# Kernel tuning notes

Measured on AMD Instinct MI355X. Metric: run time of the kernel, lower is better.

The kernel has to match this reference:

```python
import jax, jax.numpy as jnp
import numpy as np

B, L, D = 2, 2048, 512
DI, N, K, R = 1024, 16, 4, 32  # d_inner=2*d_model, d_state, d_conv, dt_rank=ceil(512/16)
CK = 31   # conformer depthwise kernel
DFF = 2048  # feedforward_factor * d_hidden

def _ln(h, g, b):
    m = h.mean(-1, keepdims=True)
    v = ((h - m) ** 2).mean(-1, keepdims=True)
    return (h - m) * jax.lax.rsqrt(v + 1e-5) * g + b

def _dwconv(h, w, b, pad):
    # h: [B,L,C], w: [C,1,K] depthwise kernel
    y = jax.lax.conv_general_dilated(h.transpose(0, 2, 1), w, (1,), [pad],
                                     feature_group_count=h.shape[-1],
                                     dimension_numbers=('NCH', 'OIH', 'NCH'))
    return y.transpose(0, 2, 1) + b

def setup_inputs():
    key = jax.random.key(0)
    ks = jax.random.split(key, 16)
    nrm = lambda k, s, sc=0.02: jax.random.normal(k, s, jnp.float32) * sc
    return {
        'x': jax.random.normal(ks[0], (B, L, D), jnp.float32),
        'ln_g': jnp.ones(D), 'ln_b': jnp.zeros(D),
        'W_in': nrm(ks[1], (D, 2 * DI)),
        'conv_w': nrm(ks[2], (DI, 1, K), 0.1), 'conv_b': jnp.zeros(DI),
        'W_x': nrm(ks[3], (DI, R + 2 * N)),
        'W_dt': nrm(ks[4], (R, DI), 0.1), 'b_dt': nrm(ks[5], (DI,), 0.1),
        'A_log': jnp.log(jnp.broadcast_to(jnp.arange(1, N + 1, dtype=jnp.float32), (DI, N))),
        'Dp': jnp.ones(DI),
        'W_out': nrm(ks[6], (DI, D)),
        'cm_ln_g': jnp.ones(D), 'cm_ln_b': jnp.zeros(D),
        'cm_pw1_w': nrm(ks[7], (D, 2 * D)), 'cm_pw1_b': jnp.zeros(2 * D),
        'cm_dw_w': nrm(ks[8], (D, 1, CK), 0.1), 'cm_dw_b': jnp.zeros(D),
        'cm_pw2_w': nrm(ks[9], (D, D)), 'cm_pw2_b': jnp.zeros(D),
        'ff_W1': nrm(ks[10], (D, DFF)), 'ff_b1': jnp.zeros(DFF),
        'ff_W2': nrm(ks[11], (DFF, D)), 'ff_b2': jnp.zeros(D),
    }

def _forward(x, ln_g, ln_b, W_in, conv_w, conv_b, W_x, W_dt, b_dt, A_log, Dp, W_out,
             cm_ln_g, cm_ln_b, cm_pw1_w, cm_pw1_b, cm_dw_w, cm_dw_b, cm_pw2_w, cm_pw2_b,
             ff_W1, ff_b1, ff_W2, ff_b2):
    # --- pre LayerNorm ---
    h = _ln(x, ln_g, ln_b)
    # --- Mamba block ---
    xz = h @ W_in                       # [B,L,2*DI]
    xi, z = xz[..., :DI], xz[..., DI:]
    xc = jax.nn.silu(_dwconv(xi, conv_w, conv_b, (K - 1, 0)))  # causal depthwise conv
    dbl = xc @ W_x                      # [B,L,R+2N]
    dt, Bm, Cm = dbl[..., :R], dbl[..., R:R + N], dbl[..., R + N:]
    delta = jax.nn.softplus(dt @ W_dt + b_dt)           # [B,L,DI]
    A = -jnp.exp(A_log)                                  # [DI,N]
    dA = jnp.exp(delta[..., None] * A)                   # [B,L,DI,N]
    dBu = (delta * xc)[..., None] * Bm[:, :, None, :]    # [B,L,DI,N]
    def step(hs, inp):
        a, bu, c = inp
        hs = a * hs + bu                                 # [B,DI,N]
        return hs, jnp.einsum('bdn,bn->bd', hs, c)
    h0 = jnp.zeros((x.shape[0], DI, N), x.dtype)
    _, ys = jax.lax.scan(step, h0, (dA.transpose(1, 0, 2, 3), dBu.transpose(1, 0, 2, 3), Cm.transpose(1, 0, 2)))
    y = ys.transpose(1, 0, 2) + Dp * xc
    y = y * jax.nn.silu(z)
    m = y @ W_out                                        # [B,L,D]
    # --- Conformer-style conv module (residual) ---
    c = _ln(m, cm_ln_g, cm_ln_b)
    c = c @ cm_pw1_w + cm_pw1_b
    a_, g_ = jnp.split(c, 2, axis=-1)
    c = a_ * jax.nn.sigmoid(g_)  # GLU
    c = jax.nn.silu(_dwconv(c, cm_dw_w, cm_dw_b, ((CK - 1) // 2, (CK - 1) // 2)))
    c = c @ cm_pw2_w + cm_pw2_b
    m = m + c
    # --- post LayerNorm (shared params) + FFN (residual) ---
    f = _ln(m, ln_g, ln_b)
    out = f + (jax.nn.gelu(f @ ff_W1 + ff_b1) @ ff_W2 + ff_b2)
    return out

def reference(x, ln_g, ln_b, W_in, conv_w, conv_b, W_x, W_dt, b_dt, A_log, Dp, W_out,
              cm_ln_g, cm_ln_b, cm_pw1_w, cm_pw1_b, cm_dw_w, cm_dw_b, cm_pw2_w, cm_pw2_b,
              ff_W1, ff_b1, ff_W2, ff_b2):
    return _forward(x, ln_g, ln_b, W_in, conv_w, conv_b, W_x, W_dt, b_dt, A_log, Dp, W_out,
                    cm_ln_g, cm_ln_b, cm_pw1_w, cm_pw1_b, cm_dw_w, cm_dw_b, cm_pw2_w, cm_pw2_b,
                    ff_W1, ff_b1, ff_W2, ff_b2)
```

## Files before the change

kernel.cpp:

```cpp
#include <hip/hip_runtime.h>
#include <hip/hip_bf16.h>
#include <math.h>

#define Bc   2
#define Lc   2048
#define Dc   512
#define DIc  1024
#define Nc   16
#define Kc   4
#define Rc   32
#define CKc  31
#define DFFc 2048
#define Mrows (Bc*Lc)
#define CHUNK  32
#define NCHUNK 64

typedef __hip_bfloat16 bf16;
typedef short bf16x8 __attribute__((ext_vector_type(8)));
typedef float f32x4  __attribute__((ext_vector_type(4)));

__device__ __forceinline__ float sigmoidf_(float x){ return 1.f/(1.f+expf(-x)); }
__device__ __forceinline__ float siluf_(float x){ return x*sigmoidf_(x); }
__device__ __forceinline__ float softplusf_(float x){ return fmaxf(x,0.f)+log1pf(expf(-fabsf(x))); }
__device__ __forceinline__ float geluf_(float x){
    float x3 = x*x*x;
    return 0.5f*x*(1.f+tanhf(0.7978845608028654f*(x+0.044715f*x3)));
}

__device__ __forceinline__ void gload16(const void* g, void* l) {
    __builtin_amdgcn_global_load_lds((const __attribute__((address_space(1))) void*)g,
                                     (__attribute__((address_space(3))) void*)l, 16, 0, 0);
}

template<bool WF, bool WB>
__global__ void ln_kernel(const float* __restrict__ in, const float* __restrict__ g,
                          const float* __restrict__ bb, float* __restrict__ outf,
                          bf16* __restrict__ outb, int D) {
    int row = blockIdx.x;
    const float* x = in + (size_t)row * D;
    float s = 0.f, s2 = 0.f;
    for (int i = threadIdx.x; i < D; i += blockDim.x) { float v = x[i]; s += v; s2 += v*v; }
    #pragma unroll
    for (int off = 32; off; off >>= 1) { s += __shfl_down(s, off); s2 += __shfl_down(s2, off); }
    __shared__ float sh[2][4];
    int wave = threadIdx.x >> 6, lane = threadIdx.x & 63;
    if (lane == 0) { sh[0][wave] = s; sh[1][wave] = s2; }
    __syncthreads();
    if (threadIdx.x == 0) {
        float ts = 0.f, ts2 = 0.f;
        int nw = blockDim.x >> 6;
        for (int w = 0; w < nw; ++w) { ts += sh[0][w]; ts2 += sh[1][w]; }
        sh[0][0] = ts; sh[1][0] = ts2;
    }
    __syncthreads();
    float mean = sh[0][0] / D;
    float var  = sh[1][0] / D - mean*mean;
    float rstd = rsqrtf(var + 1e-5f);
    for (int i = threadIdx.x; i < D; i += blockDim.x) {
        float v = (x[i]-mean)*rstd*g[i] + bb[i];
        if (WF) outf[(size_t)row*D + i] = v;
        if (WB) outb[(size_t)row*D + i] = __float2bfloat16(v);
    }
}

__global__ void wtrans(const float* __restrict__ W, bf16* __restrict__ Wt, int K, int N) {
    __shared__ float t[32][33];
    int bx = blockIdx.x, by = blockIdx.y;
    int tx = threadIdx.x, ty = threadIdx.y;
    #pragma unroll
    for (int i = 0; i < 32; i += 8)
        t[ty+i][tx] = W[(size_t)(by*32+ty+i)*N + bx*32+tx];
    __syncthreads();
    #pragma unroll
    for (int i = 0; i < 32; i += 8)
        Wt[(size_t)(bx*32+ty+i)*K + by*32+tx] = __float2bfloat16(t[tx][ty+i]);
}

template<int BM, int BN, int SPLITK, int ACT, bool BIAS, bool RES, bool WF32, bool WBF16>
__global__ __launch_bounds__(256) void mgemm(const bf16* __restrict__ A, int lda,
                                             const bf16* __restrict__ Wt,
                                             const float* __restrict__ bias,
                                             const float* __restrict__ res,
                                             float* __restrict__ outf,
                                             bf16* __restrict__ outb,
                                             int M, int N, int K) {
    constexpr int BK = 32;
    constexpr int WM = BM/2, WN = BN/2;
    constexpr int AM = WM/16, AN = WN/16;
    constexpr int AISS = BM/64, BISS = BN/64;
    __shared__ __align__(16) bf16 As[2][BM*BK];
    __shared__ __align__(16) bf16 Bs[2][BN*BK];
    const int tid  = threadIdx.x;
    const int wave = tid >> 6, lane = tid & 63;
    const int r16  = lane & 15, kb = lane >> 4;
    const int gx = gridDim.x;
    const int nwg = gx*gridDim.y;
    const int id  = blockIdx.y*gx + blockIdx.x;
    const int sid = (id & 7)*(nwg >> 3) + (id >> 3);
    const int bm = (sid / gx)*BM, bn = (sid % gx)*BN;
    const int wm = (wave>>1)*WM, wn = (wave&1)*WN;
    const int Keff = K / SPLITK;
    const int kz0  = (SPLITK > 1) ? blockIdx.z * Keff : 0;
    f32x4 acc[AM][AN] = {};
    const int nt = Keff / BK;

    auto stage = [&](int buf, int kt) {
        #pragma unroll
        for (int it = 0; it < AISS; ++it) {
            int base = (wave*AISS + it) << 10;
            int Lb   = base + (lane << 4);
            int row  = Lb >> 6;
            int gch  = ((Lb >> 4) & 3) ^ (row & 3);
            gload16(A + (size_t)(bm + row)*lda + kz0 + kt*BK + gch*8, (char*)As[buf] + base);
        }
        #pragma unroll
        for (int it = 0; it < BISS; ++it) {
            int base = (wave*BISS + it) << 10;
            int Lb   = base + (lane << 4);
            int row  = Lb >> 6;
            int gch  = ((Lb >> 4) & 3) ^ (row & 3);
            gload16(Wt + (size_t)(bn + row)*K + kz0 + kt*BK + gch*8, (char*)Bs[buf] + base);
        }
    };

    stage(0, 0);
    __syncthreads();
    for (int t = 0; t < nt; ++t) {
        int cur = t & 1;
        if (t + 1 < nt) stage(cur ^ 1, t + 1);
        bf16x8 af[AM], bfr[AN];
        #pragma unroll
        for (int mi = 0; mi < AM; ++mi) {
            int r = wm + mi*16 + r16;
            af[mi] = *(const bf16x8*)((const char*)As[cur] + r*64 + ((kb ^ (r & 3)) << 4));
        }
        #pragma unroll
        for (int ni = 0; ni < AN; ++ni) {
            int r = wn + ni*16 + r16;
            bfr[ni] = *(const bf16x8*)((const char*)Bs[cur] + r*64 + ((kb ^ (r & 3)) << 4));
        }
        #pragma unroll
        for (int mi = 0; mi < AM; ++mi)
            #pragma unroll
            for (int ni = 0; ni < AN; ++ni)
                acc[mi][ni] = __builtin_amdgcn_mfma_f32_16x16x32_bf16(af[mi], bfr[ni], acc[mi][ni], 0, 0, 0);
        __syncthreads();
    }

    #pragma unroll
    for (int mi = 0; mi < AM; ++mi) {
        #pragma unroll
        for (int ni = 0; ni < AN; ++ni) {
            #pragma unroll
            for (int r = 0; r < 4; ++r) {
                int grow = bm + wm + mi*16 + kb*4 + r;
                int gcol = bn + wn + ni*16 + r16;
                float v = acc[mi][ni][r];
                if (SPLITK > 1) {
                    outf[(size_t)blockIdx.z*M*N + (size_t)grow*N + gcol] = v;
                } else {
                    if (BIAS) v += bias[gcol];
                    if (ACT == 1) v = softplusf_(v);
                    else if (ACT == 2) v = geluf_(v);
                    if (RES) v += res[(size_t)grow*N + gcol];
                    if (WF32)  outf[(size_t)grow*N + gcol] = v;
                    if (WBF16) outb[(size_t)grow*N + gcol] = __float2bfloat16(v);
                }
            }
        }
    }
}

__global__ void splitk_combine(const float* __restrict__ part, float* __restrict__ outf,
                               bf16* __restrict__ outb, int n, int parts) {
    int i = blockIdx.x*256 + threadIdx.x;
    if (i >= n) return;
    float s = 0.f;
    for (int p = 0; p < parts; ++p) s += part[(size_t)p*n + i];
    outf[i] = s;
    outb[i] = __float2bfloat16(s);
}

template<int T>
__global__ __launch_bounds__(256) void causal_conv_silu(const float* __restrict__ xi, const float* __restrict__ w,
                                                        const float* __restrict__ bias, float* __restrict__ xc,
                                                        bf16* __restrict__ xcb) {
    int d  = blockIdx.x*256 + threadIdx.x;
    int b  = blockIdx.y;
    int l0 = blockIdx.z*T;
    const float* src = xi + (size_t)b*Lc*DIc + d;
    float wt[Kc];
    #pragma unroll
    for (int k = 0; k < Kc; ++k) wt[k] = w[d*Kc + k];
    float win[T + Kc - 1];
    #pragma unroll
    for (int i = 0; i < T + Kc - 1; ++i) {
        int li = l0 - (Kc-1) + i;
        win[i] = (li >= 0) ? src[(size_t)li*DIc] : 0.f;
    }
    float bv = bias[d];
    size_t obase = (size_t)b*Lc*DIc + (size_t)l0*DIc + d;
    #pragma unroll
    for (int o = 0; o < T; ++o) {
        float acc = bv;
        #pragma unroll
        for (int k = 0; k < Kc; ++k) acc = fmaf(win[o+k], wt[k], acc);
        float v = siluf_(acc);
        xc[obase + (size_t)o*DIc] = v;
        xcb[obase + (size_t)o*DIc] = __float2bfloat16(v);
    }
}

__global__ __launch_bounds__(256) void scan_pass1(const float* __restrict__ delta, const float* __restrict__ xc,
                                                  const float* __restrict__ dbl, const float* __restrict__ A_log,
                                                  float* __restrict__ P, float* __restrict__ H) {
    int dgroup = blockIdx.x & 3;
    int bc = blockIdx.x >> 2;
    int b = bc & 1, chunk = bc >> 1;
    int d = dgroup*256 + threadIdx.x;
    float Av[16];
    #pragma unroll
    for (int j = 0; j < 4; ++j) {
        f32x4 v = *(const f32x4*)(&A_log[d*16 + 4*j]);
        #pragma unroll
        for (int q = 0; q < 4; ++q) Av[4*j+q] = -__expf(v[q]);
    }
    float h[16], Pl[16];
    #pragma unroll
    for (int n = 0; n < 16; ++n) { h[n] = 0.f; Pl[n] = 1.f; }
    size_t row0 = (size_t)b*Lc + (size_t)chunk*CHUNK;
    for (int i = 0; i < CHUNK; ++i) {
        size_t rowi = row0 + i;
        float dv  = delta[rowi*DIc + d];
        float xcv = xc[rowi*DIc + d];
        float dxc = dv*xcv;
        f32x4 B0 = *(const f32x4*)(&dbl[rowi*64 + Rc + 0]);
        f32x4 B1 = *(const f32x4*)(&dbl[rowi*64 + Rc + 4]);
        f32x4 B2 = *(const f32x4*)(&dbl[rowi*64 + Rc + 8]);
        f32x4 B3 = *(const f32x4*)(&dbl[rowi*64 + Rc + 12]);
        float Bv[16];
        #pragma unroll
        for (int q = 0; q < 4; ++q) { Bv[q]=B0[q]; Bv[4+q]=B1[q]; Bv[8+q]=B2[q]; Bv[12+q]=B3[q]; }
        #pragma unroll
        for (int n = 0; n < 16; ++n) {
            float a = __expf(dv*Av[n]);
            h[n] = fmaf(a, h[n], dxc*Bv[n]);
            Pl[n] *= a;
        }
    }
    size_t pidx = ((size_t)chunk*2048 + (size_t)b*DIc + d) * 16;
    #pragma unroll
    for (int j = 0; j < 4; ++j) {
        f32x4 vp, vh;
        #pragma unroll
        for (int q = 0; q < 4; ++q) { vp[q] = Pl[4*j+q]; vh[q] = h[4*j+q]; }
        *(f32x4*)(&P[pidx + 4*j]) = vp;
        *(f32x4*)(&H[pidx + 4*j]) = vh;
    }
}

__global__ void scan_combine(float* __restrict__ P, const float* __restrict__ H) {
    int t = blockIdx.x*blockDim.x + threadIdx.x;
    float h = 0.f;
    #pragma unroll
    for (int c = 0; c < NCHUNK; ++c) {
        size_t idx = (size_t)c*32768 + t;
        float Pv = P[idx], Hv = H[idx];
        P[idx] = h;
        h = fmaf(Pv, h, Hv);
    }
}

__global__ __launch_bounds__(256) void scan_pass3(const float* __restrict__ delta, const float* __restrict__ xc,
                                                  const float* __restrict__ dbl, const float* __restrict__ z,
                                                  const float* __restrict__ A_log, const float* __restrict__ Dp,
                                                  const float* __restrict__ hstart, bf16* __restrict__ y) {
    int dgroup = blockIdx.x & 3;
    int bc = blockIdx.x >> 2;
    int b = bc & 1, chunk = bc >> 1;
    int d = dgroup*256 + threadIdx.x;
    float Av[16];
    #pragma unroll
    for (int j = 0; j < 4; ++j) {
        f32x4 v = *(const f32x4*)(&A_log[d*16 + 4*j]);
        #pragma unroll
        for (int q = 0; q < 4; ++q) Av[4*j+q] = -__expf(v[q]);
    }
    float Dv = Dp[d];
    float h[16];
    size_t pidx = ((size_t)chunk*2048 + (size_t)b*DIc + d) * 16;
    #pragma unroll
    for (int j = 0; j < 4; ++j) {
        f32x4 v = *(const f32x4*)(&hstart[pidx + 4*j]);
        #pragma unroll
        for (int q = 0; q < 4; ++q) h[4*j+q] = v[q];
    }
    size_t row0 = (size_t)b*Lc + (size_t)chunk*CHUNK;
    for (int i = 0; i < CHUNK; ++i) {
        size_t rowi = row0 + i;
        float dv  = delta[rowi*DIc + d];
        float xcv = xc[rowi*DIc + d];
        float dxc = dv*xcv;
        f32x4 B0 = *(const f32x4*)(&dbl[rowi*64 + Rc + 0]);
        f32x4 B1 = *(const f32x4*)(&dbl[rowi*64 + Rc + 4]);
        f32x4 B2 = *(const f32x4*)(&dbl[rowi*64 + Rc + 8]);
        f32x4 B3 = *(const f32x4*)(&dbl[rowi*64 + Rc + 12]);
        f32x4 C0 = *(const f32x4*)(&dbl[rowi*64 + Rc + Nc + 0]);
        f32x4 C1 = *(const f32x4*)(&dbl[rowi*64 + Rc + Nc + 4]);
        f32x4 C2 = *(const f32x4*)(&dbl[rowi*64 + Rc + Nc + 8]);
        f32x4 C3 = *(const f32x4*)(&dbl[rowi*64 + Rc + Nc + 12]);
        float Bv[16], Cv[16];
        #pragma unroll
        for (int q = 0; q < 4; ++q) {
            Bv[q]=B0[q]; Bv[4+q]=B1[q]; Bv[8+q]=B2[q]; Bv[12+q]=B3[q];
            Cv[q]=C0[q]; Cv[4+q]=C1[q]; Cv[8+q]=C2[q]; Cv[12+q]=C3[q];
        }
        float s0=0.f, s1=0.f, s2=0.f, s3=0.f;
        #pragma unroll
        for (int n = 0; n < 16; ++n) {
            float a = __expf(dv*Av[n]);
            h[n] = fmaf(a, h[n], dxc*Bv[n]);
        }
        #pragma unroll
        for (int j = 0; j < 4; ++j) {
            s0 = fmaf(h[4*j+0], Cv[4*j+0], s0);
            s1 = fmaf(h[4*j+1], Cv[4*j+1], s1);
            s2 = fmaf(h[4*j+2], Cv[4*j+2], s2);
            s3 = fmaf(h[4*j+3], Cv[4*j+3], s3);
        }
        float contrib = (s0+s1)+(s2+s3);
        float zv = z[rowi*DIc + d];
        y[rowi*DIc + d] = __float2bfloat16((contrib + Dv*xcv) * siluf_(zv));
    }
}

__global__ void glu_kernel(const float* __restrict__ c2, float* __restrict__ out) {
    int idx = blockIdx.x*blockDim.x + threadIdx.x;
    if (idx >= Bc*Lc*Dc) return;
    int col = idx & (Dc-1); int row = idx >> 9;
    float a  = c2[(size_t)row*(2*Dc) + col];
    float gg = c2[(size_t)row*(2*Dc) + Dc + col];
    out[idx] = a * sigmoidf_(gg);
}

template<int T>
__global__ __launch_bounds__(256) void sym_conv_silu(const float* __restrict__ in, const float* __restrict__ w,
                                                     const float* __restrict__ bias, bf16* __restrict__ out) {
    int d  = blockIdx.x*256 + threadIdx.x;
    int b  = blockIdx.y;
    int l0 = blockIdx.z*T;
    const float* src = in + (size_t)b*Lc*Dc + d;
    float wt[CKc];
    #pragma unroll
    for (int k = 0; k < CKc; ++k) wt[k] = w[d*CKc + k];
    constexpr int HALF = (CKc-1)/2;
    float win[T + CKc - 1];
    #pragma unroll
    for (int i = 0; i < T + CKc - 1; ++i) {
        int li = l0 - HALF + i;
        win[i] = (li >= 0 && li < Lc) ? src[(size_t)li*Dc] : 0.f;
    }
    float bv = bias[d];
    size_t obase = (size_t)b*Lc*Dc + (size_t)l0*Dc + d;
    #pragma unroll
    for (int o = 0; o < T; ++o) {
        float acc = bv;
        #pragma unroll
        for (int k = 0; k < CKc; ++k) acc = fmaf(win[o+k], wt[k], acc);
        out[obase + (size_t)o*Dc] = __float2bfloat16(siluf_(acc));
    }
}

extern "C" void kernel_launch(void* const* d_in, const int* in_sizes, int n_in,
                              void* d_out, int out_size, void* d_ws, size_t ws_size,
                              hipStream_t stream) {
    const float* x      = (const float*)d_in[0];
    const float* ln_g   = (const float*)d_in[1];
    const float* ln_b   = (const float*)d_in[2];
    const float* W_in   = (const float*)d_in[3];
    const float* conv_w = (const float*)d_in[4];
    const float* conv_b = (const float*)d_in[5];
    const float* W_x    = (const float*)d_in[6];
    const float* W_dt   = (const float*)d_in[7];
    const float* b_dt   = (const float*)d_in[8];
    const float* A_log  = (const float*)d_in[9];
    const float* Dp     = (const float*)d_in[10];
    const float* W_out  = (const float*)d_in[11];
    const float* cm_ln_g= (const float*)d_in[12];
    const float* cm_ln_b= (const float*)d_in[13];
    const float* pw1_w  = (const float*)d_in[14];
    const float* pw1_b  = (const float*)d_in[15];
    const float* dw_w   = (const float*)d_in[16];
    const float* dw_b   = (const float*)d_in[17];
    const float* pw2_w  = (const float*)d_in[18];
    const float* pw2_b  = (const float*)d_in[19];
    const float* ff_W1  = (const float*)d_in[20];
    const float* ff_b1  = (const float*)d_in[21];
    const float* ff_W2  = (const float*)d_in[22];
    const float* ff_b2  = (const float*)d_in[23];
    float* out = (float*)d_out;
    float* ws  = (float*)d_ws;

    float* A_  = ws;
    float* A2_ = ws + 4194304;
    float* B_  = ws + 8388608;
    float* C_  = ws + 12582912;
    float* D_  = ws + 12845056;
    float* F_  = ws + 17039360;
    float* H_  = ws + 18612224;
    float* J_  = ws + 20709376;

    float* xi_buf  = A_;
    float* part_buf= A_;
    float* P_buf   = A_;
    float* H_buf   = A_ + 2097152;
    float* c2_buf  = A_;
    float* z_buf   = A2_;
    float* glu_buf = A2_;
    float* xc_buf  = B_;
    bf16*  g1b     = (bf16*)B_;
    float* dbl_buf = C_;
    float* dl_buf  = D_;
    float* m_buf   = D_;
    bf16*  dblb    = (bf16*)F_;
    bf16*  cb      = (bf16*)F_;
    bf16*  ccb     = (bf16*)F_;
    bf16*  fb      = (bf16*)F_;
    bf16*  hb      = (bf16*)H_;
    bf16*  xcb     = (bf16*)H_;
    bf16*  yb      = (bf16*)H_;
    float* f_buf   = out;

    bf16* Jw = (bf16*)J_;
    bf16* Win_t  = Jw;
    bf16* Wx_t   = Jw + 1048576;
    bf16* Wdt_t  = Jw + 1114112;
    bf16* Wout_t = Jw + 1146880;
    bf16* pw1_t  = Jw + 1671168;
    bf16* pw2_t  = Jw + 2195456;
    bf16* ffW1_t = Jw + 2457600;
    bf16* ffW2_t = Jw + 3506176;

    const int M = Mrows;
    dim3 tw(32,8);

    wtrans<<<dim3(2048/32, 512/32), tw, 0, stream>>>(W_in,  Win_t,  512,  2048);
    wtrans<<<dim3(  64/32,1024/32), tw, 0, stream>>>(W_x,   Wx_t,   1024, 64);
    wtrans<<<dim3(1024/32,  32/32), tw, 0, stream>>>(W_dt,  Wdt_t,  32,   1024);
    wtrans<<<dim3( 512/32,1024/32), tw, 0, stream>>>(W_out, Wout_t, 1024, 512);
    wtrans<<<dim3(1024/32, 512/32), tw, 0, stream>>>(pw1_w, pw1_t,  512,  1024);
    wtrans<<<dim3( 512/32, 512/32), tw, 0, stream>>>(pw2_w, pw2_t,  512,  512);
    wtrans<<<dim3(2048/32, 512/32), tw, 0, stream>>>(ff_W1, ffW1_t, 512,  2048);
    wtrans<<<dim3( 512/32,2048/32), tw, 0, stream>>>(ff_W2, ffW2_t, 2048, 512);

    ln_kernel<false,true><<<M, 256, 0, stream>>>(x, ln_g, ln_b, nullptr, hb, Dc);
    mgemm<64,64,1,0,false,false,true,false><<<dim3(1024/64, M/64), 256, 0, stream>>>(
        hb, Dc, Win_t, nullptr, nullptr, xi_buf, nullptr, M, DIc, Dc);
    mgemm<64,64,1,0,false,false,true,false><<<dim3(1024/64, M/64), 256, 0, stream>>>(
        hb, Dc, Win_t + (size_t)DIc*Dc, nullptr, nullptr, z_buf, nullptr, M, DIc, Dc);
    causal_conv_silu<16><<<dim3(DIc/256, Bc, Lc/16), 256, 0, stream>>>(xi_buf, conv_w, conv_b, xc_buf, xcb);
    mgemm<64,64,8,0,false,false,true,false><<<dim3(64/64, M/64, 8), 256, 0, stream>>>(
        xcb, DIc, Wx_t, nullptr, nullptr, part_buf, nullptr, M, 64, DIc);
    splitk_combine<<<(M*64+255)/256, 256, 0, stream>>>(part_buf, dbl_buf, dblb, M*64, 8);
    mgemm<64,64,1,1,true,false,true,false><<<dim3(1024/64, M/64), 256, 0, stream>>>(
        dblb, 64, Wdt_t, b_dt, nullptr, dl_buf, nullptr, M, DIc, Rc);
    scan_pass1<<<512, 256, 0, stream>>>(dl_buf, xc_buf, dbl_buf, A_log, P_buf, H_buf);
    scan_combine<<<128, 256, 0, stream>>>(P_buf, H_buf);
    scan_pass3<<<512, 256, 0, stream>>>(dl_buf, xc_buf, dbl_buf, z_buf, A_log, Dp, P_buf, yb);
    mgemm<64,64,1,0,false,false,true,false><<<dim3(512/64, M/64), 256, 0, stream>>>(
        yb, DIc, Wout_t, nullptr, nullptr, m_buf, nullptr, M, Dc, DIc);
    ln_kernel<false,true><<<M, 256, 0, stream>>>(m_buf, cm_ln_g, cm_ln_b, nullptr, cb, Dc);
    mgemm<64,64,1,0,true,false,true,false><<<dim3(1024/64, M/64), 256, 0, stream>>>(
        cb, Dc, pw1_t, pw1_b, nullptr, c2_buf, nullptr, M, 2*Dc, Dc);
    glu_kernel<<<(M*Dc+255)/256, 256, 0, stream>>>(c2_buf, glu_buf);
    sym_conv_silu<16><<<dim3(Dc/256, Bc, Lc/16), 256, 0, stream>>>(glu_buf, dw_w, dw_b, ccb);
    mgemm<64,64,1,0,true,true,true,false><<<dim3(512/64, M/64), 256, 0, stream>>>(
        ccb, Dc, pw2_t, pw2_b, m_buf, m_buf, nullptr, M, Dc, Dc);
    ln_kernel<true,true><<<M, 256, 0, stream>>>(m_buf, ln_g, ln_b, f_buf, fb, Dc);
    mgemm<64,64,1,2,true,false,false,true><<<dim3(2048/64, M/64), 256, 0, stream>>>(
        fb, Dc, ffW1_t, ff_b1, nullptr, nullptr, g1b, M, DFFc, Dc);
    mgemm<64,64,1,0,true,true,true,false><<<dim3(512/64, M/64), 256, 0, stream>>>(
        g1b, DFFc, ffW2_t, ff_b2, f_buf, out, nullptr, M, Dc, DFFc);
}
```

Baseline: 261.0 us.

## Batch weight transposes, merge in_proj GEMMs, fuse GLU into conv, drop fp32 xc

All eight weight transposes now run in a single launch that looks up its matrix from a packed descriptor. The xi and z input-projection GEMMs become one launch that selects weights and output by blockIdx.z. The GLU is computed inside the depthwise conv kernel, so the separate GLU pass and its intermediate buffer are gone. The scan kernels read the bf16 copy of xc instead of an fp32 copy, which cuts launches and memory traffic at some cost in precision for the scan input.

```diff
diff --git a/kernel.cpp b/kernel.cpp
--- a/kernel.cpp
+++ b/kernel.cpp
@@ -63,9 +63,26 @@
     }
 }
 
-__global__ void wtrans(const float* __restrict__ W, bf16* __restrict__ Wt, int K, int N) {
+struct WtPack {
+    const float* W[8];
+    bf16* Wt[8];
+    int K[8];
+    int N[8];
+    int start[9];
+};
+
+__global__ void wtrans_all(WtPack p) {
     __shared__ float t[32][33];
-    int bx = blockIdx.x, by = blockIdx.y;
+    int tb = blockIdx.x;
+    int wi = 0;
+    #pragma unroll
+    for (int i = 0; i < 7; ++i) if (tb >= p.start[i+1]) wi = i+1;
+    int lt = tb - p.start[wi];
+    int K = p.K[wi], N = p.N[wi];
+    int ntx = N >> 5;
+    int bx = lt % ntx, by = lt / ntx;
+    const float* W = p.W[wi];
+    bf16* Wt = p.Wt[wi];
     int tx = threadIdx.x, ty = threadIdx.y;
     #pragma unroll
     for (int i = 0; i < 32; i += 8)
@@ -76,7 +93,7 @@
         Wt[(size_t)(bx*32+ty+i)*K + by*32+tx] = __float2bfloat16(t[tx][ty+i]);
 }
 
-template<int BM, int BN, int SPLITK, int ACT, bool BIAS, bool RES, bool WF32, bool WBF16>
+template<int BM, int BN, int SPLITK, int ZSEL, int ACT, bool BIAS, bool RES, bool WF32, bool WBF16>
 __global__ __launch_bounds__(256) void mgemm(const bf16* __restrict__ A, int lda,
                                              const bf16* __restrict__ Wt,
                                              const float* __restrict__ bias,
@@ -99,6 +116,9 @@
     const int sid = (id & 7)*(nwg >> 3) + (id >> 3);
     const int bm = (sid / gx)*BM, bn = (sid % gx)*BN;
     const int wm = (wave>>1)*WM, wn = (wave&1)*WN;
+    const bf16* Wp = Wt;
+    float* outfp = outf;
+    if (ZSEL) { Wp += (size_t)blockIdx.z*N*K; outfp += (size_t)blockIdx.z*M*N; }
     const int Keff = K / SPLITK;
     const int kz0  = (SPLITK > 1) ? blockIdx.z * Keff : 0;
     f32x4 acc[AM][AN] = {};
@@ -119,7 +139,7 @@
             int Lb   = base + (lane << 4);
             int row  = Lb >> 6;
             int gch  = ((Lb >> 4) & 3) ^ (row & 3);
-            gload16(Wt + (size_t)(bn + row)*K + kz0 + kt*BK + gch*8, (char*)Bs[buf] + base);
+            gload16(Wp + (size_t)(bn + row)*K + kz0 + kt*BK + gch*8, (char*)Bs[buf] + base);
         }
     };
 
@@ -163,7 +183,7 @@
                     if (ACT == 1) v = softplusf_(v);
                     else if (ACT == 2) v = geluf_(v);
                     if (RES) v += res[(size_t)grow*N + gcol];
-                    if (WF32)  outf[(size_t)grow*N + gcol] = v;
+                    if (WF32)  outfp[(size_t)grow*N + gcol] = v;
                     if (WBF16) outb[(size_t)grow*N + gcol] = __float2bfloat16(v);
                 }
             }
@@ -183,7 +203,7 @@
 
 template<int T>
 __global__ __launch_bounds__(256) void causal_conv_silu(const float* __restrict__ xi, const float* __restrict__ w,
-                                                        const float* __restrict__ bias, float* __restrict__ xc,
+                                                        const float* __restrict__ bias,
                                                         bf16* __restrict__ xcb) {
     int d  = blockIdx.x*256 + threadIdx.x;
     int b  = blockIdx.y;
@@ -205,13 +225,11 @@
         float acc = bv;
         #pragma unroll
         for (int k = 0; k < Kc; ++k) acc = fmaf(win[o+k], wt[k], acc);
-        float v = siluf_(acc);
-        xc[obase + (size_t)o*DIc] = v;
-        xcb[obase + (size_t)o*DIc] = __float2bfloat16(v);
-    }
-}
-
-__global__ __launch_bounds__(256) void scan_pass1(const float* __restrict__ delta, const float* __restrict__ xc,
+        xcb[obase + (size_t)o*DIc] = __float2bfloat16(siluf_(acc));
+    }
+}
+
+__global__ __launch_bounds__(256) void scan_pass1(const float* __restrict__ delta, const bf16* __restrict__ xc,
                                                   const float* __restrict__ dbl, const float* __restrict__ A_log,
                                                   float* __restrict__ P, float* __restrict__ H) {
     int dgroup = blockIdx.x & 3;
@@ -232,7 +250,7 @@
     for (int i = 0; i < CHUNK; ++i) {
         size_t rowi = row0 + i;
         float dv  = delta[rowi*DIc + d];
-        float xcv = xc[rowi*DIc + d];
+        float xcv = __bfloat162float(xc[rowi*DIc + d]);
         float dxc = dv*xcv;
         f32x4 B0 = *(const f32x4*)(&dbl[rowi*64 + Rc + 0]);
         f32x4 B1 = *(const f32x4*)(&dbl[rowi*64 + Rc + 4]);
@@ -271,7 +289,7 @@
     }
 }
 
-__global__ __launch_bounds__(256) void scan_pass3(const float* __restrict__ delta, const float* __restrict__ xc,
+__global__ __launch_bounds__(256) void scan_pass3(const float* __restrict__ delta, const bf16* __restrict__ xc,
                                                   const float* __restrict__ dbl, const float* __restrict__ z,
                                                   const float* __restrict__ A_log, const float* __restrict__ Dp,
                                                   const float* __restrict__ hstart, bf16* __restrict__ y) {
@@ -299,7 +317,7 @@
     for (int i = 0; i < CHUNK; ++i) {
         size_t rowi = row0 + i;
         float dv  = delta[rowi*DIc + d];
-        float xcv = xc[rowi*DIc + d];
+        float xcv = __bfloat162float(xc[rowi*DIc + d]);
         float dxc = dv*xcv;
         f32x4 B0 = *(const f32x4*)(&dbl[rowi*64 + Rc + 0]);
         f32x4 B1 = *(const f32x4*)(&dbl[rowi*64 + Rc + 4]);
@@ -334,22 +352,13 @@
     }
 }
 
-__global__ void glu_kernel(const float* __restrict__ c2, float* __restrict__ out) {
-    int idx = blockIdx.x*blockDim.x + threadIdx.x;
-    if (idx >= Bc*Lc*Dc) return;
-    int col = idx & (Dc-1); int row = idx >> 9;
-    float a  = c2[(size_t)row*(2*Dc) + col];
-    float gg = c2[(size_t)row*(2*Dc) + Dc + col];
-    out[idx] = a * sigmoidf_(gg);
-}
-
 template<int T>
-__global__ __launch_bounds__(256) void sym_conv_silu(const float* __restrict__ in, const float* __restrict__ w,
-                                                     const float* __restrict__ bias, bf16* __restrict__ out) {
+__global__ __launch_bounds__(256) void sym_conv_glu_silu(const float* __restrict__ c2, const float* __restrict__ w,
+                                                         const float* __restrict__ bias, bf16* __restrict__ out) {
     int d  = blockIdx.x*256 + threadIdx.x;
     int b  = blockIdx.y;
     int l0 = blockIdx.z*T;
-    const float* src = in + (size_t)b*Lc*Dc + d;
+    const float* base = c2 + (size_t)b*Lc*(2*Dc) + d;
     float wt[CKc];
     #pragma unroll
     for (int k = 0; k < CKc; ++k) wt[k] = w[d*CKc + k];
@@ -358,7 +367,11 @@
     #pragma unroll
     for (int i = 0; i < T + CKc - 1; ++i) {
         int li = l0 - HALF + i;
-        win[i] = (li >= 0 && li < Lc) ? src[(size_t)li*Dc] : 0.f;
+        if (li >= 0 && li < Lc) {
+            float a = base[(size_t)li*(2*Dc)];
+            float g = base[(size_t)li*(2*Dc) + Dc];
+            win[i] = a * sigmoidf_(g);
+        } else win[i] = 0.f;
     }
     float bv = bias[d];
     size_t obase = (size_t)b*Lc*Dc + (size_t)l0*Dc + d;
@@ -416,8 +429,6 @@
     float* H_buf   = A_ + 2097152;
     float* c2_buf  = A_;
     float* z_buf   = A2_;
-    float* glu_buf = A2_;
-    float* xc_buf  = B_;
     bf16*  g1b     = (bf16*)B_;
     float* dbl_buf = C_;
     float* dl_buf  = D_;
@@ -442,43 +453,46 @@
     bf16* ffW2_t = Jw + 3506176;
 
     const int M = Mrows;
-    dim3 tw(32,8);
-
-    wtrans<<<dim3(2048/32, 512/32), tw, 0, stream>>>(W_in,  Win_t,  512,  2048);
-    wtrans<<<dim3(  64/32,1024/32), tw, 0, stream>>>(W_x,   Wx_t,   1024, 64);
-    wtrans<<<dim3(1024/32,  32/32), tw, 0, stream>>>(W_dt,  Wdt_t,  32,   1024);
-    wtrans<<<dim3( 512/32,1024/32), tw, 0, stream>>>(W_out, Wout_t, 1024, 512);
-    wtrans<<<dim3(1024/32, 512/32), tw, 0, stream>>>(pw1_w, pw1_t,  512,  1024);
-    wtrans<<<dim3( 512/32, 512/32), tw, 0, stream>>>(pw2_w, pw2_t,  512,  512);
-    wtrans<<<dim3(2048/32, 512/32), tw, 0, stream>>>(ff_W1, ffW1_t, 512,  2048);
-    wtrans<<<dim3( 512/32,2048/32), tw, 0, stream>>>(ff_W2, ffW2_t, 2048, 512);
+
+    {
+        WtPack p;
+        const float* Ws[8] = {W_in, W_x, W_dt, W_out, pw1_w, pw2_w, ff_W1, ff_W2};
+        bf16* Ts[8] = {Win_t, Wx_t, Wdt_t, Wout_t, pw1_t, pw2_t, ffW1_t, ffW2_t};
+        int Ks[8] = {512, 1024, 32, 1024, 512, 512, 512, 2048};
+        int Ns[8] = {2048, 64, 1024, 512, 1024, 512, 2048, 512};
+        int acc = 0;
+        for (int i = 0; i < 8; ++i) {
+            p.W[i] = Ws[i]; p.Wt[i] = Ts[i]; p.K[i] = Ks[i]; p.N[i] = Ns[i];
+            p.start[i] = acc;
+            acc += (Ns[i]/32)*(Ks[i]/32);
+        }
+        p.start[8] = acc;
+        wtrans_all<<<acc, dim3(32,8), 0, stream>>>(p);
+    }
 
     ln_kernel<false,true><<<M, 256, 0, stream>>>(x, ln_g, ln_b, nullptr, hb, Dc);
-    mgemm<64,64,1,0,false,false,true,false><<<dim3(1024/64, M/64), 256, 0, stream>>>(
+    mgemm<64,64,1,1,0,false,false,true,false><<<dim3(1024/64, M/64, 2), 256, 0, stream>>>(
         hb, Dc, Win_t, nullptr, nullptr, xi_buf, nullptr, M, DIc, Dc);
-    mgemm<64,64,1,0,false,false,true,false><<<dim3(1024/64, M/64), 256, 0, stream>>>(
-        hb, Dc, Win_t + (size_t)DIc*Dc, nullptr, nullptr, z_buf, nullptr, M, DIc, Dc);
-    causal_conv_silu<16><<<dim3(DIc/256, Bc, Lc/16), 256, 0, stream>>>(xi_buf, conv_w, conv_b, xc_buf, xcb);
-    mgemm<64,64,8,0,false,false,true,false><<<dim3(64/64, M/64, 8), 256, 0, stream>>>(
+    causal_conv_silu<16><<<dim3(DIc/256, Bc, Lc/16), 256, 0, stream>>>(xi_buf, conv_w, conv_b, xcb);
+    mgemm<64,64,8,0,0,false,false,true,false><<<dim3(64/64, M/64, 8), 256, 0, stream>>>(
         xcb, DIc, Wx_t, nullptr, nullptr, part_buf, nullptr, M, 64, DIc);
     splitk_combine<<<(M*64+255)/256, 256, 0, stream>>>(part_buf, dbl_buf, dblb, M*64, 8);
-    mgemm<64,64,1,1,true,false,true,false><<<dim3(1024/64, M/64), 256, 0, stream>>>(
+    mgemm<64,64,1,0,1,true,false,true,false><<<dim3(1024/64, M/64), 256, 0, stream>>>(
         dblb, 64, Wdt_t, b_dt, nullptr, dl_buf, nullptr, M, DIc, Rc);
-    scan_pass1<<<512, 256, 0, stream>>>(dl_buf, xc_buf, dbl_buf, A_log, P_buf, H_buf);
+    scan_pass1<<<512, 256, 0, stream>>>(dl_buf, xcb, dbl_buf, A_log, P_buf, H_buf);
     scan_combine<<<128, 256, 0, stream>>>(P_buf, H_buf);
-    scan_pass3<<<512, 256, 0, stream>>>(dl_buf, xc_buf, dbl_buf, z_buf, A_log, Dp, P_buf, yb);
-    mgemm<64,64,1,0,false,false,true,false><<<dim3(512/64, M/64), 256, 0, stream>>>(
+    scan_pass3<<<512, 256, 0, stream>>>(dl_buf, xcb, dbl_buf, z_buf, A_log, Dp, P_buf, yb);
+    mgemm<64,64,1,0,0,false,false,true,false><<<dim3(512/64, M/64), 256, 0, stream>>>(
         yb, DIc, Wout_t, nullptr, nullptr, m_buf, nullptr, M, Dc, DIc);
     ln_kernel<false,true><<<M, 256, 0, stream>>>(m_buf, cm_ln_g, cm_ln_b, nullptr, cb, Dc);
-    mgemm<64,64,1,0,true,false,true,false><<<dim3(1024/64, M/64), 256, 0, stream>>>(
+    mgemm<64,64,1,0,0,true,false,true,false><<<dim3(1024/64, M/64), 256, 0, stream>>>(
         cb, Dc, pw1_t, pw1_b, nullptr, c2_buf, nullptr, M, 2*Dc, Dc);
-    glu_kernel<<<(M*Dc+255)/256, 256, 0, stream>>>(c2_buf, glu_buf);
-    sym_conv_silu<16><<<dim3(Dc/256, Bc, Lc/16), 256, 0, stream>>>(glu_buf, dw_w, dw_b, ccb);
-    mgemm<64,64,1,0,true,true,true,false><<<dim3(512/64, M/64), 256, 0, stream>>>(
+    sym_conv_glu_silu<16><<<dim3(Dc/256, Bc, Lc/16), 256, 0, stream>>>(c2_buf, dw_w, dw_b, ccb);
+    mgemm<64,64,1,0,0,true,true,true,false><<<dim3(512/64, M/64), 256, 0, stream>>>(
         ccb, Dc, pw2_t, pw2_b, m_buf, m_buf, nullptr, M, Dc, Dc);
     ln_kernel<true,true><<<M, 256, 0, stream>>>(m_buf, ln_g, ln_b, f_buf, fb, Dc);
-    mgemm<64,64,1,2,true,false,false,true><<<dim3(2048/64, M/64), 256, 0, stream>>>(
+    mgemm<64,64,1,0,2,true,false,false,true><<<dim3(2048/64, M/64), 256, 0, stream>>>(
         fb, Dc, ffW1_t, ff_b1, nullptr, nullptr, g1b, M, DFFc, Dc);
-    mgemm<64,64,1,0,true,true,true,false><<<dim3(512/64, M/64), 256, 0, stream>>>(
+    mgemm<64,64,1,0,0,true,true,true,false><<<dim3(512/64, M/64), 256, 0, stream>>>(
         g1b, DFFc, ffW2_t, ff_b2, f_buf, out, nullptr, M, Dc, DFFc);
 }
```

Measured after the change: 251.0 us. 1.04x faster.
